# Optimization experiments

Measured on AMD Instinct MI355X. Metric: run time of the kernel, lower is better.

The kernel has to match this reference:

```python
import jax, jax.numpy as jnp
import numpy as np

ALPHA = 1.0
BETA = 0.5
LOSS_WEIGHT = 1.0


def setup_inputs() -> dict:
    key = jax.random.key(0)
    k1, k2 = jax.random.split(key)
    pred = jax.random.normal(k1, (16384, 4), dtype=jnp.float32)
    target = jax.random.normal(k2, (16384, 4), dtype=jnp.float32)
    return {"pred": pred, "target": target}


def reference(pred, target):
    # pred: (N,4) xyz + polarity; target: (M,4)
    pred_xyz = pred[:, :3]
    target_xyz = target[:, :3]
    pred_p = pred[:, 3:4]          # (N,1)
    target_p = target[None, :, 3]  # (1,M)

    # squared euclidean distance via norm expansion (avoids N x M x 3 tensor)
    pn = jnp.sum(pred_xyz * pred_xyz, axis=1, keepdims=True)      # (N,1)
    tn = jnp.sum(target_xyz * target_xyz, axis=1, keepdims=True)  # (M,1)
    cross = pred_xyz @ target_xyz.T                               # (N,M)
    dist_xyz = jnp.maximum(pn + tn.T - 2.0 * cross, 0.0)

    dist_p = (pred_p - target_p) ** 2                             # (N,M)
    combined = ALPHA * dist_xyz + BETA * dist_p

    min_p2g = jnp.min(combined, axis=1)
    min_g2p = jnp.min(combined, axis=0)
    chamfer = jnp.mean(min_p2g) + jnp.mean(min_g2p)
    return chamfer * LOSS_WEIGHT
```

## Files before the change

kernel.cpp:

```cpp
#include <hip/hip_runtime.h>

#define NPTS   16384
#define RPB    256
#define CPB    512
#define NRB    (NPTS / RPB)
#define NCB    (NPTS / CPB)

typedef short  bf16x8 __attribute__((ext_vector_type(8)));
typedef float  f32x16 __attribute__((ext_vector_type(16)));

__device__ __forceinline__ unsigned rne_bf16(float f) {
    unsigned u = __float_as_uint(f);
    return (u + 0x7fffu + ((u >> 16) & 1u)) >> 16;
}
__device__ __forceinline__ float bf16_dec(unsigned h) {
    return __uint_as_float(h << 16);
}
#define ONE_BF 0x3f80u

__device__ __forceinline__ float tree16_min(f32x16 a) {
    float x0 = fminf(fminf(a[0],  a[1]),  a[2]);
    float x1 = fminf(fminf(a[3],  a[4]),  a[5]);
    float x2 = fminf(fminf(a[6],  a[7]),  a[8]);
    float x3 = fminf(fminf(a[9],  a[10]), a[11]);
    float x4 = fminf(fminf(a[12], a[13]), a[14]);
    float y0 = fminf(fminf(x0, x1), x2);
    float y1 = fminf(fminf(x3, x4), a[15]);
    return fminf(y0, y1);
}


__global__ __launch_bounds__(256) void prep_kernel(
    const float4* __restrict__ pred, const float4* __restrict__ tgt,
    uint4* __restrict__ wpred, uint4* __restrict__ ptgt,
    unsigned int* __restrict__ minbuf)
{
    int i = blockIdx.x * 256 + threadIdx.x;
    if (i >= NPTS) return;

    minbuf[i]        = 0x7f7f7f7fu;
    minbuf[i + NPTS] = 0x7f7f7f7fu;

    unsigned onepk = ONE_BF | (ONE_BF << 16);

    {
        float4 v = pred[i];
        float n = fmaf(v.x, v.x, fmaf(v.y, v.y, fmaf(v.z, v.z, 0.5f * v.w * v.w)));
        unsigned nh = rne_bf16(n);
        unsigned nl = rne_bf16(n - bf16_dec(nh));
        unsigned npk = nh | (nl << 16);
        float w0 = -2.0f * v.x, w1 = -2.0f * v.y, w2 = -2.0f * v.z, w3 = -v.w;
        unsigned h0 = rne_bf16(w0), h1 = rne_bf16(w1), h2 = rne_bf16(w2), h3 = rne_bf16(w3);
        unsigned l0 = rne_bf16(w0 - bf16_dec(h0)), l1 = rne_bf16(w1 - bf16_dec(h1));
        unsigned l2 = rne_bf16(w2 - bf16_dec(h2)), l3 = rne_bf16(w3 - bf16_dec(h3));
        wpred[i * 2 + 0] = make_uint4(h0 | (h1 << 16), h2 | (h3 << 16),
                                      l0 | (l1 << 16), l2 | (l3 << 16));
        wpred[i * 2 + 1] = make_uint4(h0 | (h1 << 16), h2 | (h3 << 16),
                                      onepk, npk);
    }
    {
        float4 v = tgt[i];
        float n = fmaf(v.x, v.x, fmaf(v.y, v.y, fmaf(v.z, v.z, 0.5f * v.w * v.w)));
        unsigned nh = rne_bf16(n);
        unsigned nl = rne_bf16(n - bf16_dec(nh));
        unsigned npk = nh | (nl << 16);
        unsigned g0 = rne_bf16(v.x), g1 = rne_bf16(v.y), g2 = rne_bf16(v.z), g3 = rne_bf16(v.w);
        unsigned m0 = rne_bf16(v.x - bf16_dec(g0)), m1 = rne_bf16(v.y - bf16_dec(g1));
        unsigned m2 = rne_bf16(v.z - bf16_dec(g2)), m3 = rne_bf16(v.w - bf16_dec(g3));
        ptgt[i * 2 + 0] = make_uint4(g0 | (g1 << 16), g2 | (g3 << 16),
                                     g0 | (g1 << 16), g2 | (g3 << 16));
        ptgt[i * 2 + 1] = make_uint4(m0 | (m1 << 16), m2 | (m3 << 16),
                                     npk, onepk);
    }
}

__global__ __launch_bounds__(256, 4) void chamfer_mfma_kernel(
    const bf16x8* __restrict__ wpred, const bf16x8* __restrict__ ptgt,
    unsigned int* __restrict__ minbuf)
{
    __shared__ unsigned colLds[CPB];
    __shared__ float red[RPB];

    for (int c = threadIdx.x; c < CPB; c += 256) colLds[c] = 0x7f7f7f7fu;
    __syncthreads();

    const int lane = threadIdx.x & 63;
    const int wave = threadIdx.x >> 6;
    const int half = lane >> 5;
    const int lid  = lane & 31;

    const int rowBase = blockIdx.x * RPB + wave * 64;
    const int colBase = blockIdx.y * CPB;

    bf16x8 a0 = wpred[(rowBase +      lid) * 2 + half];
    bf16x8 a1 = wpred[(rowBase + 32 + lid) * 2 + half];

    float mr0[16], mr1[16];
#pragma unroll
    for (int r = 0; r < 16; ++r) { mr0[r] = 3.0e38f; mr1[r] = 3.0e38f; }

    const bf16x8* bp = ptgt + (colBase + lid) * 2 + half;
    const f32x16 kZero = (f32x16)(0.0f);

#pragma unroll 2
    for (int t = 0; t < CPB / 64; ++t) {
        bf16x8 b0 = bp[t * 128];
        bf16x8 b1 = bp[t * 128 + 64];

        f32x16 A0 = __builtin_amdgcn_mfma_f32_32x32x16_bf16(a0, b0, kZero, 0, 0, 0);
        f32x16 A1 = __builtin_amdgcn_mfma_f32_32x32x16_bf16(a0, b1, kZero, 0, 0, 0);
#pragma unroll
        for (int r = 0; r < 16; ++r)
            mr0[r] = fminf(fminf(A0[r], A1[r]), mr0[r]);
        float ta = tree16_min(A0);
        float tb = tree16_min(A1);
        __builtin_amdgcn_sched_barrier(0x20);

        f32x16 B0 = __builtin_amdgcn_mfma_f32_32x32x16_bf16(a1, b0, kZero, 0, 0, 0);
        f32x16 B1 = __builtin_amdgcn_mfma_f32_32x32x16_bf16(a1, b1, kZero, 0, 0, 0);
#pragma unroll
        for (int r = 0; r < 16; ++r)
            mr1[r] = fminf(fminf(B0[r], B1[r]), mr1[r]);
        ta = fminf(ta, tree16_min(B0));
        tb = fminf(tb, tree16_min(B1));
        __builtin_amdgcn_sched_barrier(0x20);

        atomicMin(&colLds[t * 64 +      lid], __float_as_uint(fmaxf(ta, 0.0f)));
        atomicMin(&colLds[t * 64 + 32 + lid], __float_as_uint(fmaxf(tb, 0.0f)));
    }

#pragma unroll
    for (int r = 0; r < 16; ++r) {
        float v0 = mr0[r], v1 = mr1[r];
        v0 = fminf(v0, __shfl_xor(v0, 16)); v1 = fminf(v1, __shfl_xor(v1, 16));
        v0 = fminf(v0, __shfl_xor(v0, 8));  v1 = fminf(v1, __shfl_xor(v1, 8));
        v0 = fminf(v0, __shfl_xor(v0, 4));  v1 = fminf(v1, __shfl_xor(v1, 4));
        v0 = fminf(v0, __shfl_xor(v0, 2));  v1 = fminf(v1, __shfl_xor(v1, 2));
        v0 = fminf(v0, __shfl_xor(v0, 1));  v1 = fminf(v1, __shfl_xor(v1, 1));
        if (lid == 0) {
            int row = (r & 3) + 8 * (r >> 2) + 4 * half;
            red[wave * 64 + row]      = v0;
            red[wave * 64 + 32 + row] = v1;
        }
    }
    __syncthreads();

    {
        float v = fmaxf(red[threadIdx.x], 0.0f);
        atomicMin(&minbuf[blockIdx.x * RPB + threadIdx.x], __float_as_uint(v));
    }
#pragma unroll
    for (int s = 0; s < 2; ++s) {
        int c = threadIdx.x + s * 256;
        atomicMin(&minbuf[NPTS + colBase + c], colLds[c]);
    }
}

__global__ __launch_bounds__(1024) void chamfer_reduce_kernel(
    const unsigned int* __restrict__ minbuf, float* __restrict__ out)
{
    __shared__ float red[16];
    const uint4* mb4 = (const uint4*)minbuf;
    float s = 0.0f;
#pragma unroll
    for (int it = 0; it < (2 * NPTS / 4) / 1024; ++it) {
        uint4 u = mb4[it * 1024 + threadIdx.x];
        s += __uint_as_float(u.x) + __uint_as_float(u.y)
           + __uint_as_float(u.z) + __uint_as_float(u.w);
    }
#pragma unroll
    for (int off = 32; off > 0; off >>= 1)
        s += __shfl_down(s, off);
    const int wave = threadIdx.x >> 6;
    const int lane = threadIdx.x & 63;
    if (lane == 0) red[wave] = s;
    __syncthreads();
    if (threadIdx.x == 0) {
        float t = 0.0f;
#pragma unroll
        for (int w = 0; w < 16; ++w) t += red[w];
        out[0] = t * (1.0f / (float)NPTS);
    }
}

extern "C" void kernel_launch(void* const* d_in, const int* in_sizes, int n_in,
                              void* d_out, int out_size, void* d_ws, size_t ws_size,
                              hipStream_t stream) {
    const float4* pred = (const float4*)d_in[0];
    const float4* tgt  = (const float4*)d_in[1];

    unsigned int* minbuf = (unsigned int*)d_ws;
    uint4* wpred = (uint4*)((char*)d_ws + 2 * NPTS * 4);
    uint4* ptgt  = wpred + 2 * NPTS;

    prep_kernel<<<NPTS / 256, 256, 0, stream>>>(pred, tgt, wpred, ptgt, minbuf);

    dim3 grid(NRB, NCB);
    chamfer_mfma_kernel<<<grid, 256, 0, stream>>>(
        (const bf16x8*)wpred, (const bf16x8*)ptgt, minbuf);

    chamfer_reduce_kernel<<<1, 1024, 0, stream>>>(minbuf, (float*)d_out);
}
```

Measured before the change: 36.14 us.

## Replace global atomicMin with per-block partial buffers and two-stage reduction

Each tile block now writes its row and column minima to dedicated partial arrays instead of doing global atomicMin into a shared buffer, which also removes the minbuf initialization in prep. A new multi-block reduce kernel takes the min across the 32 or 64 partials and sums per block, and a tiny finalize kernel adds those sums. This is meant to remove global atomic contention and the single-block serial reduction. The cost is about 6 MB of extra partial-buffer traffic and one additional kernel launch.

```diff
diff --git a/kernel.cpp b/kernel.cpp
--- a/kernel.cpp
+++ b/kernel.cpp
@@ -32,14 +32,10 @@
 
 __global__ __launch_bounds__(256) void prep_kernel(
     const float4* __restrict__ pred, const float4* __restrict__ tgt,
-    uint4* __restrict__ wpred, uint4* __restrict__ ptgt,
-    unsigned int* __restrict__ minbuf)
+    uint4* __restrict__ wpred, uint4* __restrict__ ptgt)
 {
     int i = blockIdx.x * 256 + threadIdx.x;
     if (i >= NPTS) return;
-
-    minbuf[i]        = 0x7f7f7f7fu;
-    minbuf[i + NPTS] = 0x7f7f7f7fu;
 
     unsigned onepk = ONE_BF | (ONE_BF << 16);
 
@@ -76,7 +72,8 @@
 
 __global__ __launch_bounds__(256, 4) void chamfer_mfma_kernel(
     const bf16x8* __restrict__ wpred, const bf16x8* __restrict__ ptgt,
-    unsigned int* __restrict__ minbuf)
+    float* __restrict__ rowpart,
+    float* __restrict__ colpart)
 {
     __shared__ unsigned colLds[CPB];
     __shared__ float red[RPB];
@@ -145,42 +142,49 @@
     }
     __syncthreads();
 
-    {
-        float v = fmaxf(red[threadIdx.x], 0.0f);
-        atomicMin(&minbuf[blockIdx.x * RPB + threadIdx.x], __float_as_uint(v));
-    }
+    rowpart[blockIdx.y * NPTS + blockIdx.x * RPB + threadIdx.x] =
+        fmaxf(red[threadIdx.x], 0.0f);
 #pragma unroll
     for (int s = 0; s < 2; ++s) {
         int c = threadIdx.x + s * 256;
-        atomicMin(&minbuf[NPTS + colBase + c], colLds[c]);
-    }
-}
-
-__global__ __launch_bounds__(1024) void chamfer_reduce_kernel(
-    const unsigned int* __restrict__ minbuf, float* __restrict__ out)
-{
-    __shared__ float red[16];
-    const uint4* mb4 = (const uint4*)minbuf;
-    float s = 0.0f;
-#pragma unroll
-    for (int it = 0; it < (2 * NPTS / 4) / 1024; ++it) {
-        uint4 u = mb4[it * 1024 + threadIdx.x];
-        s += __uint_as_float(u.x) + __uint_as_float(u.y)
-           + __uint_as_float(u.z) + __uint_as_float(u.w);
-    }
-#pragma unroll
-    for (int off = 32; off > 0; off >>= 1)
-        s += __shfl_down(s, off);
-    const int wave = threadIdx.x >> 6;
-    const int lane = threadIdx.x & 63;
-    if (lane == 0) red[wave] = s;
+        colpart[blockIdx.x * NPTS + colBase + c] = __uint_as_float(colLds[c]);
+    }
+}
+
+__global__ __launch_bounds__(256) void reduce1_kernel(
+    const float* __restrict__ rowpart, const float* __restrict__ colpart,
+    float* __restrict__ partsum)
+{
+    const int b = blockIdx.x, t = threadIdx.x;
+    float m;
+    if (b < 64) {
+        int r = b * 256 + t;
+        m = rowpart[r];
+#pragma unroll
+        for (int k = 1; k < NCB; ++k) m = fminf(m, rowpart[k * NPTS + r]);
+    } else {
+        int c = (b - 64) * 256 + t;
+        m = colpart[c];
+#pragma unroll
+        for (int k = 1; k < NRB; ++k) m = fminf(m, colpart[k * NPTS + c]);
+    }
+    float s = m;
+#pragma unroll
+    for (int off = 32; off > 0; off >>= 1) s += __shfl_down(s, off);
+    __shared__ float red[4];
+    if ((t & 63) == 0) red[t >> 6] = s;
     __syncthreads();
-    if (threadIdx.x == 0) {
-        float t = 0.0f;
-#pragma unroll
-        for (int w = 0; w < 16; ++w) t += red[w];
-        out[0] = t * (1.0f / (float)NPTS);
-    }
+    if (t == 0) partsum[b] = red[0] + red[1] + red[2] + red[3];
+}
+
+__global__ __launch_bounds__(64) void finalize_kernel(
+    const float* __restrict__ partsum, float* __restrict__ out)
+{
+    const int t = threadIdx.x;
+    float s = partsum[t] + partsum[t + 64];
+#pragma unroll
+    for (int off = 32; off > 0; off >>= 1) s += __shfl_down(s, off);
+    if (t == 0) out[0] = s * (1.0f / (float)NPTS);
 }
 
 extern "C" void kernel_launch(void* const* d_in, const int* in_sizes, int n_in,
@@ -189,15 +193,19 @@
     const float4* pred = (const float4*)d_in[0];
     const float4* tgt  = (const float4*)d_in[1];
 
-    unsigned int* minbuf = (unsigned int*)d_ws;
-    uint4* wpred = (uint4*)((char*)d_ws + 2 * NPTS * 4);
-    uint4* ptgt  = wpred + 2 * NPTS;
-
-    prep_kernel<<<NPTS / 256, 256, 0, stream>>>(pred, tgt, wpred, ptgt, minbuf);
+    char* ws = (char*)d_ws;
+    float* rowpart = (float*)ws;
+    float* colpart = (float*)(ws + (2u << 20));
+    float* partsum = (float*)(ws + (6u << 20));
+    uint4* wpred   = (uint4*)(ws + (6u << 20) + 4096);
+    uint4* ptgt    = wpred + 2 * NPTS;
+
+    prep_kernel<<<NPTS / 256, 256, 0, stream>>>(pred, tgt, wpred, ptgt);
 
     dim3 grid(NRB, NCB);
     chamfer_mfma_kernel<<<grid, 256, 0, stream>>>(
-        (const bf16x8*)wpred, (const bf16x8*)ptgt, minbuf);
-
-    chamfer_reduce_kernel<<<1, 1024, 0, stream>>>(minbuf, (float*)d_out);
-}
+        (const bf16x8*)wpred, (const bf16x8*)ptgt, rowpart, colpart);
+
+    reduce1_kernel<<<128, 256, 0, stream>>>(rowpart, colpart, partsum);
+    finalize_kernel<<<1, 64, 0, stream>>>(partsum, (float*)d_out);
+}
```

Result: slower. 38.63 us (+6.9%).
